# Kernel optimization log

Measured on AMD Instinct MI355X. Metric: run time of the kernel, lower is better.

Reference implementation:

```python
import jax, jax.numpy as jnp
import numpy as np


def _conv1d(x, w, b, stride=1, pad=0):
    # x: [B, Cin, L], w: [Cout, Cin, K] (torch OIH layout)
    y = jax.lax.conv_general_dilated(
        x, w, window_strides=(stride,), padding=[(pad, pad)],
        dimension_numbers=('NCH', 'OIH', 'NCH'))
    return y + b[None, :, None]


def setup_inputs() -> dict:
    key = jax.random.key(0)
    ks = jax.random.split(key, 8)
    B, M, C, Hf, Wf, Ho, Wo = 4, 112, 512, 13, 13, 16, 16
    return {
        'features_f': jax.random.normal(ks[0], (B, C, Hf, Wf), jnp.float32),   # cfp last feature map
        'oct_feats':  jax.random.normal(ks[1], (B, M, C, Ho, Wo), jnp.float32),  # per-slice last feature maps
        'conv1d_w':   jax.random.normal(ks[2], (64, 1024, 64), jnp.float32) * 0.02,
        'conv1d_b':   jnp.zeros((64,), jnp.float32),
        'convf_w':    jax.random.normal(ks[3], (13, 64, 5), jnp.float32) * 0.05,
        'convf_b':    jnp.zeros((13,), jnp.float32),
        'head_w':     jax.random.normal(ks[4], (3, 1536), jnp.float32) * 0.02,
        'head_b':     jnp.zeros((3,), jnp.float32),
    }


def reference(features_f, oct_feats, conv1d_w, conv1d_b, convf_w, convf_b, head_w, head_b):
    B, M, C, Ho, Wo = oct_feats.shape
    # per-slice global avg / max pools of encoder_o feature maps -> [B, M, C]
    fv = oct_feats.mean(axis=(3, 4))
    fv_max = oct_feats.max(axis=(3, 4))
    # slice attention: conv1d over slice axis on concatenated [B, 2C, M]
    x = jnp.concatenate([fv, fv_max], axis=2).transpose(0, 2, 1)
    slice_weights = jax.nn.sigmoid(_conv1d(x, conv1d_w, conv1d_b))  # [B, 64, M-63]
    # argmax-indexed per-channel gather: for each (b, c) pick the slice whose
    # pooled activation is largest, then copy that slice's [Ho, Wo] map.
    idx = jnp.argmax(fv, axis=1)          # [B, C]
    idx_max = jnp.argmax(fv_max, axis=1)  # [B, C]
    sel = jnp.take_along_axis(oct_feats, idx[:, None, :, None, None], axis=1)[:, 0]        # [B, C, Ho, Wo]
    sel_max = jnp.take_along_axis(oct_feats, idx_max[:, None, :, None, None], axis=1)[:, 0]
    feat_o_avg = sel.mean(axis=(2, 3))      # original applies avgpool to both selections
    feat_o_max = sel_max.mean(axis=(2, 3))
    feat_o = jnp.concatenate([feat_o_avg, feat_o_max], axis=1)  # [B, 1024]
    # fundus attention map r: [B, 13, 13], broadcast over C channels
    r = jax.nn.sigmoid(_conv1d(slice_weights, convf_w, convf_b, stride=4, pad=2))
    attended = features_f + r[:, None, :, :] * features_f
    feat_f = attended.mean(axis=(2, 3))     # [B, 512]
    feat = jnp.concatenate([feat_f, feat_o], axis=1)  # [B, 1536]
    # classification head (dropout is identity at inference): Linear(1536 -> 3)
    return feat @ head_w.T + head_b
```

## Files before the change

kernel.cpp:

```cpp
#include <hip/hip_runtime.h>
#include <hip/hip_bf16.h>
#include <math.h>

#define XB_OFF 0
#define FO_OFF 917504
#define AM_OFF 933888
#define SW_OFF 933888
#define RF_OFF 0
#define FT_OFF 933888

__global__ __launch_bounds__(256) void k_init(unsigned long long* __restrict__ am) {
    am[blockIdx.x * 256 + threadIdx.x] = 0ULL;
}

__global__ __launch_bounds__(256) void k_pool(const float* __restrict__ oct,
                                              __hip_bfloat16* __restrict__ xb,
                                              unsigned long long* __restrict__ am) {
    int wg = (blockIdx.x * 256 + threadIdx.x) >> 6;
    int lane = threadIdx.x & 63;
    const float4* p = (const float4*)(oct + (size_t)wg * 256);
    float4 v = p[lane];
    float s  = v.x + v.y + v.z + v.w;
    float mx = fmaxf(fmaxf(v.x, v.y), fmaxf(v.z, v.w));
#pragma unroll
    for (int off = 32; off >= 1; off >>= 1) {
        s  += __shfl_xor(s, off);
        mx  = fmaxf(mx, __shfl_xor(mx, off));
    }
    if (lane == 0) {
        int c  = wg & 511;
        int bm = wg >> 9;
        int m  = bm % 112;
        int b  = bm / 112;
        xb[((size_t)b * 1024 + c) * 112 + m]       = __float2bfloat16(s * (1.0f / 256.0f));
        xb[((size_t)b * 1024 + 512 + c) * 112 + m] = __float2bfloat16(mx);
        unsigned int u = __float_as_uint(mx);
        unsigned int key = (u & 0x80000000u) ? ~u : (u | 0x80000000u);
        unsigned long long pk = ((unsigned long long)key << 32) | (unsigned int)(111 - m);
        atomicMax(&am[b * 512 + c], pk);
    }
}

__global__ __launch_bounds__(256) void k_feato(const __hip_bfloat16* __restrict__ xb,
                                               const unsigned long long* __restrict__ am,
                                               float* __restrict__ fo) {
    int wid  = blockIdx.x * 4 + (threadIdx.x >> 6);
    int lane = threadIdx.x & 63;
    int b = wid >> 9, c = wid & 511;
    const __hip_bfloat16* fvrow = xb + ((size_t)b * 1024 + c) * 112;
    float v0 = (lane < 112)      ? __bfloat162float(fvrow[lane])      : -INFINITY;
    float v1 = (lane + 64 < 112) ? __bfloat162float(fvrow[lane + 64]) : -INFINITY;
    float mxf = fmaxf(v0, v1);
#pragma unroll
    for (int off = 32; off >= 1; off >>= 1)
        mxf = fmaxf(mxf, __shfl_xor(mxf, off));
    if (lane == 0) {
        int mstar = 111 - (int)(unsigned int)(am[b * 512 + c] & 0xFFFFFFFFULL);
        fo[b * 1024 + c]       = mxf;
        fo[b * 1024 + 512 + c] = __bfloat162float(fvrow[mstar]);
    }
}

__global__ __launch_bounds__(256) void k_conv(const __hip_bfloat16* __restrict__ xb,
                                              const float* __restrict__ w1,
                                              const float* __restrict__ b1,
                                              float* __restrict__ sw) {
    __shared__ unsigned int xs[256 * 61];
    __shared__ float red[4][25];
    int bx = blockIdx.x;
    int lh = bx & 1, co = (bx >> 1) & 63, b = bx >> 7;
    int t = threadIdx.x, wv = t >> 6, lane = t & 63;
    int l0u = lh * 12;
    float acc[25];
#pragma unroll
    for (int i = 0; i < 25; i++) acc[i] = 0.f;
    const unsigned int* gxb = (const unsigned int*)xb;
    for (int chunk = 0; chunk < 4; chunk++) {
        __syncthreads();
        for (int r = wv; r < 256; r += 4)
            if (lane < 56)
                xs[r * 61 + lane] = gxb[((size_t)b * 1024 + chunk * 256 + r) * 56 + lane];
        __syncthreads();
        int cil = wv * 64 + lane;
        int ci  = chunk * 256 + cil;
        const unsigned int* xu = xs + cil * 61 + l0u;
        float xf[88];
#pragma unroll
        for (int i = 0; i < 44; i++) {
            unsigned int u = xu[i];
            xf[2 * i]     = __uint_as_float(u << 16);
            xf[2 * i + 1] = __uint_as_float(u & 0xffff0000u);
        }
        const float* wrow = w1 + ((size_t)co * 1024 + ci) * 64;
#pragma unroll
        for (int kc = 0; kc < 4; kc++) {
            float ww[16];
#pragma unroll
            for (int j = 0; j < 16; j++) ww[j] = wrow[kc * 16 + j];
#pragma unroll
            for (int k = 0; k < 16; k++)
#pragma unroll
                for (int i = 0; i < 25; i++)
                    acc[i] += ww[k] * xf[kc * 16 + k + i];
        }
    }
#pragma unroll
    for (int i = 0; i < 25; i++) {
#pragma unroll
        for (int off = 32; off >= 1; off >>= 1)
            acc[i] += __shfl_xor(acc[i], off);
    }
    if (lane < 25) red[wv][lane] = acc[lane];
    __syncthreads();
    if (t < 25) {
        float s = red[0][t] + red[1][t] + red[2][t] + red[3][t] + b1[co];
        float sg = 1.f / (1.f + expf(-s));
        int l = lh * 24 + t;
        if (!(lh == 1 && t == 0))
            sw[(size_t)(b * 64 + co) * 49 + l] = sg;
    }
}

__global__ __launch_bounds__(256) void k_r(const float* __restrict__ sw,
                                           const float* __restrict__ cw,
                                           const float* __restrict__ cb,
                                           float* __restrict__ rf) {
    __shared__ float swl[3136];
    __shared__ float cwl[4160];
    int b = blockIdx.x, t = threadIdx.x;
    for (int i = t; i < 3136; i += 256) swl[i] = sw[b * 3136 + i];
    for (int i = t; i < 4160; i += 256) cwl[i] = cw[i];
    __syncthreads();
    if (t < 169) {
        int o = t / 13, l = t % 13;
        float s = cb[o];
        for (int i = 0; i < 64; i++) {
#pragma unroll
            for (int k = 0; k < 5; k++) {
                int pos = 4 * l + k - 2;
                if (pos >= 0 && pos < 49)
                    s += swl[i * 49 + pos] * cwl[(o * 64 + i) * 5 + k];
            }
        }
        rf[b * 169 + t] = 1.f + 1.f / (1.f + expf(-s));
    }
}

__global__ __launch_bounds__(256) void k_ff(const float* __restrict__ ff,
                                            const float* __restrict__ rf,
                                            float* __restrict__ feat) {
    __shared__ float r1[169];
    int b = blockIdx.x >> 3, cg = blockIdx.x & 7;
    int t = threadIdx.x, wv = t >> 6, lane = t & 63;
    if (t < 169) r1[t] = rf[b * 169 + t];
    __syncthreads();
#pragma unroll
    for (int j = 0; j < 16; j++) {
        int c = cg * 64 + wv * 16 + j;
        const float* row = ff + ((size_t)b * 512 + c) * 169;
        float s = row[lane] * r1[lane];
        if (lane + 64 < 169)  s += row[lane + 64]  * r1[lane + 64];
        if (lane + 128 < 169) s += row[lane + 128] * r1[lane + 128];
#pragma unroll
        for (int off = 32; off >= 1; off >>= 1) s += __shfl_xor(s, off);
        if (lane == 0) feat[b * 512 + c] = s * (1.0f / 169.0f);
    }
}

__global__ __launch_bounds__(256) void k_head(const float* __restrict__ feat,
                                              const float* __restrict__ fo,
                                              const float* __restrict__ hw,
                                              const float* __restrict__ hb,
                                              float* __restrict__ out) {
    __shared__ float red[4];
    int bj = blockIdx.x;
    int b = bj / 3, j = bj % 3;
    int t = threadIdx.x, wv = t >> 6, lane = t & 63;
    float s = 0.f;
#pragma unroll
    for (int rep = 0; rep < 6; rep++) {
        int i = rep * 256 + t;
        float fv = (i < 512) ? feat[b * 512 + i] : fo[b * 1024 + (i - 512)];
        s += fv * hw[j * 1536 + i];
    }
#pragma unroll
    for (int off = 32; off >= 1; off >>= 1) s += __shfl_xor(s, off);
    if (lane == 0) red[wv] = s;
    __syncthreads();
    if (t == 0)
        out[b * 3 + j] = red[0] + red[1] + red[2] + red[3] + hb[j];
}

extern "C" void kernel_launch(void* const* d_in, const int* in_sizes, int n_in,
                              void* d_out, int out_size, void* d_ws, size_t ws_size,
                              hipStream_t stream) {
    const float* ff  = (const float*)d_in[0];
    const float* oct = (const float*)d_in[1];
    const float* w1  = (const float*)d_in[2];
    const float* b1  = (const float*)d_in[3];
    const float* cw  = (const float*)d_in[4];
    const float* cb  = (const float*)d_in[5];
    const float* hw  = (const float*)d_in[6];
    const float* hb  = (const float*)d_in[7];
    float* out = (float*)d_out;
    char* ws = (char*)d_ws;
    __hip_bfloat16*     xb = (__hip_bfloat16*)(ws + XB_OFF);
    float*              fo = (float*)(ws + FO_OFF);
    unsigned long long* am = (unsigned long long*)(ws + AM_OFF);
    float*              sw = (float*)(ws + SW_OFF);
    float*              rf = (float*)(ws + RF_OFF);
    float*            feat = (float*)(ws + FT_OFF);

    hipLaunchKernelGGL(k_init,  dim3(8),     dim3(256), 0, stream, am);
    hipLaunchKernelGGL(k_pool,  dim3(57344), dim3(256), 0, stream, oct, xb, am);
    hipLaunchKernelGGL(k_feato, dim3(512),   dim3(256), 0, stream, xb, am, fo);
    hipLaunchKernelGGL(k_conv,  dim3(512),   dim3(256), 0, stream, xb, w1, b1, sw);
    hipLaunchKernelGGL(k_r,     dim3(4),     dim3(256), 0, stream, sw, cw, cb, rf);
    hipLaunchKernelGGL(k_ff,    dim3(32),    dim3(256), 0, stream, ff, rf, feat);
    hipLaunchKernelGGL(k_head,  dim3(12),    dim3(256), 0, stream, feat, fo, hw, hb, out);
}
```

Measured before the change: 466.4 us.

## Fuse pooling with argmax selection and merge tail kernels into one

Pooling now runs one block per (batch, channel) that loops over all slices, computing mean/max pools and the argmax-selected features in-block. This removes the atomic packed argmax, the init kernel and the separate selection kernel. The fundus attention, weighted feature pooling and linear head are fused into a single per-batch kernel. The aim is fewer launches and less atomic and intermediate traffic. The cost is a tail kernel running on only 4 blocks with strided per-thread loops.

```diff
diff --git a/kernel.cpp b/kernel.cpp
--- a/kernel.cpp
+++ b/kernel.cpp
@@ -4,61 +4,76 @@
 
 #define XB_OFF 0
 #define FO_OFF 917504
-#define AM_OFF 933888
 #define SW_OFF 933888
-#define RF_OFF 0
-#define FT_OFF 933888
-
-__global__ __launch_bounds__(256) void k_init(unsigned long long* __restrict__ am) {
-    am[blockIdx.x * 256 + threadIdx.x] = 0ULL;
-}
 
 __global__ __launch_bounds__(256) void k_pool(const float* __restrict__ oct,
                                               __hip_bfloat16* __restrict__ xb,
-                                              unsigned long long* __restrict__ am) {
-    int wg = (blockIdx.x * 256 + threadIdx.x) >> 6;
-    int lane = threadIdx.x & 63;
-    const float4* p = (const float4*)(oct + (size_t)wg * 256);
-    float4 v = p[lane];
-    float s  = v.x + v.y + v.z + v.w;
-    float mx = fmaxf(fmaxf(v.x, v.y), fmaxf(v.z, v.w));
-#pragma unroll
-    for (int off = 32; off >= 1; off >>= 1) {
-        s  += __shfl_xor(s, off);
-        mx  = fmaxf(mx, __shfl_xor(mx, off));
-    }
-    if (lane == 0) {
-        int c  = wg & 511;
-        int bm = wg >> 9;
-        int m  = bm % 112;
-        int b  = bm / 112;
-        xb[((size_t)b * 1024 + c) * 112 + m]       = __float2bfloat16(s * (1.0f / 256.0f));
-        xb[((size_t)b * 1024 + 512 + c) * 112 + m] = __float2bfloat16(mx);
-        unsigned int u = __float_as_uint(mx);
-        unsigned int key = (u & 0x80000000u) ? ~u : (u | 0x80000000u);
-        unsigned long long pk = ((unsigned long long)key << 32) | (unsigned int)(111 - m);
-        atomicMax(&am[b * 512 + c], pk);
-    }
-}
-
-__global__ __launch_bounds__(256) void k_feato(const __hip_bfloat16* __restrict__ xb,
-                                               const unsigned long long* __restrict__ am,
-                                               float* __restrict__ fo) {
-    int wid  = blockIdx.x * 4 + (threadIdx.x >> 6);
-    int lane = threadIdx.x & 63;
-    int b = wid >> 9, c = wid & 511;
-    const __hip_bfloat16* fvrow = xb + ((size_t)b * 1024 + c) * 112;
-    float v0 = (lane < 112)      ? __bfloat162float(fvrow[lane])      : -INFINITY;
-    float v1 = (lane + 64 < 112) ? __bfloat162float(fvrow[lane + 64]) : -INFINITY;
-    float mxf = fmaxf(v0, v1);
-#pragma unroll
-    for (int off = 32; off >= 1; off >>= 1)
-        mxf = fmaxf(mxf, __shfl_xor(mxf, off));
-    if (lane == 0) {
-        int mstar = 111 - (int)(unsigned int)(am[b * 512 + c] & 0xFFFFFFFFULL);
-        fo[b * 1024 + c]       = mxf;
-        fo[b * 1024 + 512 + c] = __bfloat162float(fvrow[mstar]);
-    }
+                                              float* __restrict__ fo) {
+    __shared__ unsigned int fvu[56];
+    __shared__ unsigned int fvmu[56];
+    __shared__ float s_bmx[4], s_bat[4], s_bfv[4];
+    __shared__ int   s_bm[4];
+    __hip_bfloat16* fvl  = (__hip_bfloat16*)fvu;
+    __hip_bfloat16* fvml = (__hip_bfloat16*)fvmu;
+    int b = blockIdx.x >> 9, c = blockIdx.x & 511;
+    int t = threadIdx.x, w = t >> 6, lane = t & 63;
+    int g = lane >> 4, p = lane & 15;
+    const float* base = oct + ((size_t)b * 112 * 512 + c) * 256;
+    float bmx = -INFINITY, bat = 0.f, bfv = -INFINITY;
+    int bm = 0;
+    for (int it = 0; it < 7; ++it) {
+        int m = w * 28 + it * 4 + g;
+        const float4* mp = (const float4*)(base + (size_t)m * (512 * 256));
+        float4 a0 = mp[p];
+        float4 a1 = mp[p + 16];
+        float4 a2 = mp[p + 32];
+        float4 a3 = mp[p + 48];
+        float s = (a0.x + a0.y + a0.z + a0.w) + (a1.x + a1.y + a1.z + a1.w)
+                + (a2.x + a2.y + a2.z + a2.w) + (a3.x + a3.y + a3.z + a3.w);
+        float mx = fmaxf(fmaxf(fmaxf(a0.x, a0.y), fmaxf(a0.z, a0.w)),
+                         fmaxf(fmaxf(a1.x, a1.y), fmaxf(a1.z, a1.w)));
+        mx = fmaxf(mx, fmaxf(fmaxf(fmaxf(a2.x, a2.y), fmaxf(a2.z, a2.w)),
+                             fmaxf(fmaxf(a3.x, a3.y), fmaxf(a3.z, a3.w))));
+#pragma unroll
+        for (int off = 1; off <= 8; off <<= 1) {
+            s  += __shfl_xor(s, off);
+            mx  = fmaxf(mx, __shfl_xor(mx, off));
+        }
+        float fv = s * (1.0f / 256.0f);
+        if (mx > bmx) { bmx = mx; bm = m; bat = fv; }
+        bfv = fmaxf(bfv, fv);
+        if (p == 0) {
+            fvl[m]  = __float2bfloat16(fv);
+            fvml[m] = __float2bfloat16(mx);
+        }
+    }
+#pragma unroll
+    for (int off = 16; off <= 32; off <<= 1) {
+        float omx = __shfl_xor(bmx, off);
+        int   om  = __shfl_xor(bm, off);
+        float oat = __shfl_xor(bat, off);
+        float obf = __shfl_xor(bfv, off);
+        if (omx > bmx || (omx == bmx && om < bm)) { bmx = omx; bm = om; bat = oat; }
+        bfv = fmaxf(bfv, obf);
+    }
+    if (lane == 0) { s_bmx[w] = bmx; s_bm[w] = bm; s_bat[w] = bat; s_bfv[w] = bfv; }
+    __syncthreads();
+    if (t == 0) {
+        float M = s_bmx[0], A = s_bat[0], F = s_bfv[0];
+        int   I = s_bm[0];
+        for (int w2 = 1; w2 < 4; ++w2) {
+            if (s_bmx[w2] > M || (s_bmx[w2] == M && s_bm[w2] < I)) {
+                M = s_bmx[w2]; I = s_bm[w2]; A = s_bat[w2];
+            }
+            F = fmaxf(F, s_bfv[w2]);
+        }
+        fo[b * 1024 + c]       = F;
+        fo[b * 1024 + 512 + c] = A;
+    }
+    unsigned int* xo  = (unsigned int*)(xb + (size_t)(b * 1024 + c) * 112);
+    unsigned int* xo2 = (unsigned int*)(xb + (size_t)(b * 1024 + 512 + c) * 112);
+    if (t < 56)                    xo[t]       = fvu[t];
+    else if (t >= 64 && t < 120)   xo2[t - 64] = fvmu[t - 64];
 }
 
 __global__ __launch_bounds__(256) void k_conv(const __hip_bfloat16* __restrict__ xb,
@@ -121,13 +136,20 @@
     }
 }
 
-__global__ __launch_bounds__(256) void k_r(const float* __restrict__ sw,
-                                           const float* __restrict__ cw,
-                                           const float* __restrict__ cb,
-                                           float* __restrict__ rf) {
+__global__ __launch_bounds__(256) void k_tail(const float* __restrict__ sw,
+                                              const float* __restrict__ cw,
+                                              const float* __restrict__ cb,
+                                              const float* __restrict__ ff,
+                                              const float* __restrict__ fo,
+                                              const float* __restrict__ hw,
+                                              const float* __restrict__ hb,
+                                              float* __restrict__ out) {
     __shared__ float swl[3136];
     __shared__ float cwl[4160];
-    int b = blockIdx.x, t = threadIdx.x;
+    __shared__ float rfl[169];
+    __shared__ float ffl[512];
+    __shared__ float hred[3][4];
+    int b = blockIdx.x, t = threadIdx.x, w = t >> 6, lane = t & 63;
     for (int i = t; i < 3136; i += 256) swl[i] = sw[b * 3136 + i];
     for (int i = t; i < 4160; i += 256) cwl[i] = cw[i];
     __syncthreads();
@@ -142,53 +164,43 @@
                     s += swl[i * 49 + pos] * cwl[(o * 64 + i) * 5 + k];
             }
         }
-        rf[b * 169 + t] = 1.f + 1.f / (1.f + expf(-s));
-    }
-}
-
-__global__ __launch_bounds__(256) void k_ff(const float* __restrict__ ff,
-                                            const float* __restrict__ rf,
-                                            float* __restrict__ feat) {
-    __shared__ float r1[169];
-    int b = blockIdx.x >> 3, cg = blockIdx.x & 7;
-    int t = threadIdx.x, wv = t >> 6, lane = t & 63;
-    if (t < 169) r1[t] = rf[b * 169 + t];
-    __syncthreads();
-#pragma unroll
-    for (int j = 0; j < 16; j++) {
-        int c = cg * 64 + wv * 16 + j;
-        const float* row = ff + ((size_t)b * 512 + c) * 169;
-        float s = row[lane] * r1[lane];
-        if (lane + 64 < 169)  s += row[lane + 64]  * r1[lane + 64];
-        if (lane + 128 < 169) s += row[lane + 128] * r1[lane + 128];
-#pragma unroll
-        for (int off = 32; off >= 1; off >>= 1) s += __shfl_xor(s, off);
-        if (lane == 0) feat[b * 512 + c] = s * (1.0f / 169.0f);
-    }
-}
-
-__global__ __launch_bounds__(256) void k_head(const float* __restrict__ feat,
-                                              const float* __restrict__ fo,
-                                              const float* __restrict__ hw,
-                                              const float* __restrict__ hb,
-                                              float* __restrict__ out) {
-    __shared__ float red[4];
-    int bj = blockIdx.x;
-    int b = bj / 3, j = bj % 3;
-    int t = threadIdx.x, wv = t >> 6, lane = t & 63;
-    float s = 0.f;
-#pragma unroll
-    for (int rep = 0; rep < 6; rep++) {
-        int i = rep * 256 + t;
-        float fv = (i < 512) ? feat[b * 512 + i] : fo[b * 1024 + (i - 512)];
-        s += fv * hw[j * 1536 + i];
-    }
-#pragma unroll
-    for (int off = 32; off >= 1; off >>= 1) s += __shfl_xor(s, off);
-    if (lane == 0) red[wv] = s;
-    __syncthreads();
-    if (t == 0)
-        out[b * 3 + j] = red[0] + red[1] + red[2] + red[3] + hb[j];
+        rfl[t] = 1.f + 1.f / (1.f + expf(-s));
+    }
+    __syncthreads();
+    {
+        float acc1 = 0.f, acc2 = 0.f;
+        const float* r1 = ff + ((size_t)b * 512 + t) * 169;
+        const float* r2 = r1 + 256 * 169;
+        for (int pidx = 0; pidx < 169; ++pidx) {
+            float rv = rfl[pidx];
+            acc1 += r1[pidx] * rv;
+            acc2 += r2[pidx] * rv;
+        }
+        ffl[t]       = acc1 * (1.0f / 169.0f);
+        ffl[t + 256] = acc2 * (1.0f / 169.0f);
+    }
+    __syncthreads();
+    {
+        float s0 = 0.f, s1 = 0.f, s2 = 0.f;
+#pragma unroll
+        for (int rep = 0; rep < 6; ++rep) {
+            int i = rep * 256 + t;
+            float fv = (i < 512) ? ffl[i] : fo[b * 1024 + (i - 512)];
+            s0 += fv * hw[i];
+            s1 += fv * hw[1536 + i];
+            s2 += fv * hw[3072 + i];
+        }
+#pragma unroll
+        for (int off = 32; off >= 1; off >>= 1) {
+            s0 += __shfl_xor(s0, off);
+            s1 += __shfl_xor(s1, off);
+            s2 += __shfl_xor(s2, off);
+        }
+        if (lane == 0) { hred[0][w] = s0; hred[1][w] = s1; hred[2][w] = s2; }
+    }
+    __syncthreads();
+    if (t < 3)
+        out[b * 3 + t] = hred[t][0] + hred[t][1] + hred[t][2] + hred[t][3] + hb[t];
 }
 
 extern "C" void kernel_launch(void* const* d_in, const int* in_sizes, int n_in,
@@ -204,18 +216,11 @@
     const float* hb  = (const float*)d_in[7];
     float* out = (float*)d_out;
     char* ws = (char*)d_ws;
-    __hip_bfloat16*     xb = (__hip_bfloat16*)(ws + XB_OFF);
-    float*              fo = (float*)(ws + FO_OFF);
-    unsigned long long* am = (unsigned long long*)(ws + AM_OFF);
-    float*              sw = (float*)(ws + SW_OFF);
-    float*              rf = (float*)(ws + RF_OFF);
-    float*            feat = (float*)(ws + FT_OFF);
-
-    hipLaunchKernelGGL(k_init,  dim3(8),     dim3(256), 0, stream, am);
-    hipLaunchKernelGGL(k_pool,  dim3(57344), dim3(256), 0, stream, oct, xb, am);
-    hipLaunchKernelGGL(k_feato, dim3(512),   dim3(256), 0, stream, xb, am, fo);
-    hipLaunchKernelGGL(k_conv,  dim3(512),   dim3(256), 0, stream, xb, w1, b1, sw);
-    hipLaunchKernelGGL(k_r,     dim3(4),     dim3(256), 0, stream, sw, cw, cb, rf);
-    hipLaunchKernelGGL(k_ff,    dim3(32),    dim3(256), 0, stream, ff, rf, feat);
-    hipLaunchKernelGGL(k_head,  dim3(12),    dim3(256), 0, stream, feat, fo, hw, hb, out);
-}
+    __hip_bfloat16* xb = (__hip_bfloat16*)(ws + XB_OFF);
+    float*          fo = (float*)(ws + FO_OFF);
+    float*          sw = (float*)(ws + SW_OFF);
+
+    hipLaunchKernelGGL(k_pool, dim3(2048), dim3(256), 0, stream, oct, xb, fo);
+    hipLaunchKernelGGL(k_conv, dim3(512),  dim3(256), 0, stream, xb, w1, b1, sw);
+    hipLaunchKernelGGL(k_tail, dim3(4),    dim3(256), 0, stream, sw, cw, cb, ff, fo, hw, hb, out);
+}
```

Result: slower. 476.1 us (+2.1%).

## Replace atomic argmax pooling with spilled pooled values and fuse tail kernels

Applied to the files above, without the earlier changes.

The pooling pass now writes both per-slice pooled values to workspace in fp32. A second kernel does a per-(b,c) wavefront argmax over the 112 slices, which replaces the atomic-based argmax and its init kernel. The r-map, fundus feature reduction and linear head are merged into one 4-block tail kernel, cutting two launches and the global round-trips between them. The cost is extra workspace traffic and a tail whose per-thread strided reads of the fundus features are uncoalesced and spread over only 4 blocks.

```diff
diff --git a/kernel.cpp b/kernel.cpp
--- a/kernel.cpp
+++ b/kernel.cpp
@@ -2,12 +2,70 @@
 #include <hip/hip_bf16.h>
 #include <math.h>
 
-#define XB_OFF 0
-#define FO_OFF 917504
-#define AM_OFF 933888
-#define SW_OFF 933888
-#define RF_OFF 0
-#define FT_OFF 933888
+#define XB_OFF  0
+#define FO_OFF  917504
+#define AM_OFF  933888
+#define SW_OFF  933888
+#define FVX_OFF 984064
+#define FVA_OFF 1901568
+#define SPILL_NEED (FVA_OFF + 917504)
+
+__global__ __launch_bounds__(256) void k_pool1(const float* __restrict__ oct,
+                                               __hip_bfloat16* __restrict__ xb,
+                                               float* __restrict__ fvx,
+                                               float* __restrict__ fva) {
+    int wg = (blockIdx.x * 256 + threadIdx.x) >> 6;
+    int lane = threadIdx.x & 63;
+    const float4* p = (const float4*)(oct + (size_t)wg * 256);
+    float4 v = p[lane];
+    float s  = v.x + v.y + v.z + v.w;
+    float mx = fmaxf(fmaxf(v.x, v.y), fmaxf(v.z, v.w));
+#pragma unroll
+    for (int off = 32; off >= 1; off >>= 1) {
+        s  += __shfl_xor(s, off);
+        mx  = fmaxf(mx, __shfl_xor(mx, off));
+    }
+    if (lane == 0) {
+        int c  = wg & 511;
+        int bm = wg >> 9;
+        int m  = bm % 112;
+        int b  = bm / 112;
+        float fv = s * (1.0f / 256.0f);
+        xb[((size_t)b * 1024 + c) * 112 + m]       = __float2bfloat16(fv);
+        xb[((size_t)b * 1024 + 512 + c) * 112 + m] = __float2bfloat16(mx);
+        fvx[((size_t)b * 512 + c) * 112 + m] = mx;
+        fva[((size_t)b * 512 + c) * 112 + m] = fv;
+    }
+}
+
+__global__ __launch_bounds__(256) void k_pool2(const float* __restrict__ fvx,
+                                               const float* __restrict__ fva,
+                                               float* __restrict__ fo) {
+    int wid  = blockIdx.x * 4 + (threadIdx.x >> 6);
+    int lane = threadIdx.x & 63;
+    int b = wid >> 9, c = wid & 511;
+    const float* kx = fvx + (size_t)wid * 112;
+    const float* va = fva + (size_t)wid * 112;
+    int m0 = lane, m1 = lane + 64;
+    float k0 = (m0 < 112) ? kx[m0] : -INFINITY;
+    float k1 = (m1 < 112) ? kx[m1] : -INFINITY;
+    float f0 = (m0 < 112) ? va[m0] : -INFINITY;
+    float f1 = (m1 < 112) ? va[m1] : -INFINITY;
+    float bk; int bm;
+    if (k1 > k0) { bk = k1; bm = m1; } else { bk = k0; bm = m0; }
+    float bf = fmaxf(f0, f1);
+#pragma unroll
+    for (int off = 32; off >= 1; off >>= 1) {
+        float ok = __shfl_xor(bk, off);
+        int   om = __shfl_xor(bm, off);
+        if (ok > bk || (ok == bk && om < bm)) { bk = ok; bm = om; }
+        bf = fmaxf(bf, __shfl_xor(bf, off));
+    }
+    if (lane == 0) {
+        fo[b * 1024 + c]       = bf;
+        fo[b * 1024 + 512 + c] = va[bm];
+    }
+}
 
 __global__ __launch_bounds__(256) void k_init(unsigned long long* __restrict__ am) {
     am[blockIdx.x * 256 + threadIdx.x] = 0ULL;
@@ -121,13 +179,20 @@
     }
 }
 
-__global__ __launch_bounds__(256) void k_r(const float* __restrict__ sw,
-                                           const float* __restrict__ cw,
-                                           const float* __restrict__ cb,
-                                           float* __restrict__ rf) {
+__global__ __launch_bounds__(256) void k_tail(const float* __restrict__ sw,
+                                              const float* __restrict__ cw,
+                                              const float* __restrict__ cb,
+                                              const float* __restrict__ ff,
+                                              const float* __restrict__ fo,
+                                              const float* __restrict__ hw,
+                                              const float* __restrict__ hb,
+                                              float* __restrict__ out) {
     __shared__ float swl[3136];
     __shared__ float cwl[4160];
-    int b = blockIdx.x, t = threadIdx.x;
+    __shared__ float rfl[169];
+    __shared__ float ffl[512];
+    __shared__ float hred[3][4];
+    int b = blockIdx.x, t = threadIdx.x, w = t >> 6, lane = t & 63;
     for (int i = t; i < 3136; i += 256) swl[i] = sw[b * 3136 + i];
     for (int i = t; i < 4160; i += 256) cwl[i] = cw[i];
     __syncthreads();
@@ -142,53 +207,43 @@
                     s += swl[i * 49 + pos] * cwl[(o * 64 + i) * 5 + k];
             }
         }
-        rf[b * 169 + t] = 1.f + 1.f / (1.f + expf(-s));
-    }
-}
-
-__global__ __launch_bounds__(256) void k_ff(const float* __restrict__ ff,
-                                            const float* __restrict__ rf,
-                                            float* __restrict__ feat) {
-    __shared__ float r1[169];
-    int b = blockIdx.x >> 3, cg = blockIdx.x & 7;
-    int t = threadIdx.x, wv = t >> 6, lane = t & 63;
-    if (t < 169) r1[t] = rf[b * 169 + t];
-    __syncthreads();
-#pragma unroll
-    for (int j = 0; j < 16; j++) {
-        int c = cg * 64 + wv * 16 + j;
-        const float* row = ff + ((size_t)b * 512 + c) * 169;
-        float s = row[lane] * r1[lane];
-        if (lane + 64 < 169)  s += row[lane + 64]  * r1[lane + 64];
-        if (lane + 128 < 169) s += row[lane + 128] * r1[lane + 128];
-#pragma unroll
-        for (int off = 32; off >= 1; off >>= 1) s += __shfl_xor(s, off);
-        if (lane == 0) feat[b * 512 + c] = s * (1.0f / 169.0f);
-    }
-}
-
-__global__ __launch_bounds__(256) void k_head(const float* __restrict__ feat,
-                                              const float* __restrict__ fo,
-                                              const float* __restrict__ hw,
-                                              const float* __restrict__ hb,
-                                              float* __restrict__ out) {
-    __shared__ float red[4];
-    int bj = blockIdx.x;
-    int b = bj / 3, j = bj % 3;
-    int t = threadIdx.x, wv = t >> 6, lane = t & 63;
-    float s = 0.f;
-#pragma unroll
-    for (int rep = 0; rep < 6; rep++) {
-        int i = rep * 256 + t;
-        float fv = (i < 512) ? feat[b * 512 + i] : fo[b * 1024 + (i - 512)];
-        s += fv * hw[j * 1536 + i];
-    }
-#pragma unroll
-    for (int off = 32; off >= 1; off >>= 1) s += __shfl_xor(s, off);
-    if (lane == 0) red[wv] = s;
-    __syncthreads();
-    if (t == 0)
-        out[b * 3 + j] = red[0] + red[1] + red[2] + red[3] + hb[j];
+        rfl[t] = 1.f + 1.f / (1.f + expf(-s));
+    }
+    __syncthreads();
+    {
+        float acc1 = 0.f, acc2 = 0.f;
+        const float* r1 = ff + ((size_t)b * 512 + t) * 169;
+        const float* r2 = r1 + 256 * 169;
+        for (int pidx = 0; pidx < 169; ++pidx) {
+            float rv = rfl[pidx];
+            acc1 += r1[pidx] * rv;
+            acc2 += r2[pidx] * rv;
+        }
+        ffl[t]       = acc1 * (1.0f / 169.0f);
+        ffl[t + 256] = acc2 * (1.0f / 169.0f);
+    }
+    __syncthreads();
+    {
+        float s0 = 0.f, s1 = 0.f, s2 = 0.f;
+#pragma unroll
+        for (int rep = 0; rep < 6; ++rep) {
+            int i = rep * 256 + t;
+            float fv = (i < 512) ? ffl[i] : fo[b * 1024 + (i - 512)];
+            s0 += fv * hw[i];
+            s1 += fv * hw[1536 + i];
+            s2 += fv * hw[3072 + i];
+        }
+#pragma unroll
+        for (int off = 32; off >= 1; off >>= 1) {
+            s0 += __shfl_xor(s0, off);
+            s1 += __shfl_xor(s1, off);
+            s2 += __shfl_xor(s2, off);
+        }
+        if (lane == 0) { hred[0][w] = s0; hred[1][w] = s1; hred[2][w] = s2; }
+    }
+    __syncthreads();
+    if (t < 3)
+        out[b * 3 + t] = hred[t][0] + hred[t][1] + hred[t][2] + hred[t][3] + hb[t];
 }
 
 extern "C" void kernel_launch(void* const* d_in, const int* in_sizes, int n_in,
@@ -208,14 +263,17 @@
     float*              fo = (float*)(ws + FO_OFF);
     unsigned long long* am = (unsigned long long*)(ws + AM_OFF);
     float*              sw = (float*)(ws + SW_OFF);
-    float*              rf = (float*)(ws + RF_OFF);
-    float*            feat = (float*)(ws + FT_OFF);
-
-    hipLaunchKernelGGL(k_init,  dim3(8),     dim3(256), 0, stream, am);
-    hipLaunchKernelGGL(k_pool,  dim3(57344), dim3(256), 0, stream, oct, xb, am);
-    hipLaunchKernelGGL(k_feato, dim3(512),   dim3(256), 0, stream, xb, am, fo);
-    hipLaunchKernelGGL(k_conv,  dim3(512),   dim3(256), 0, stream, xb, w1, b1, sw);
-    hipLaunchKernelGGL(k_r,     dim3(4),     dim3(256), 0, stream, sw, cw, cb, rf);
-    hipLaunchKernelGGL(k_ff,    dim3(32),    dim3(256), 0, stream, ff, rf, feat);
-    hipLaunchKernelGGL(k_head,  dim3(12),    dim3(256), 0, stream, feat, fo, hw, hb, out);
-}
+
+    if (ws_size >= (size_t)SPILL_NEED) {
+        float* fvx = (float*)(ws + FVX_OFF);
+        float* fva = (float*)(ws + FVA_OFF);
+        hipLaunchKernelGGL(k_pool1, dim3(57344), dim3(256), 0, stream, oct, xb, fvx, fva);
+        hipLaunchKernelGGL(k_pool2, dim3(512),   dim3(256), 0, stream, fvx, fva, fo);
+    } else {
+        hipLaunchKernelGGL(k_init,  dim3(8),     dim3(256), 0, stream, am);
+        hipLaunchKernelGGL(k_pool,  dim3(57344), dim3(256), 0, stream, oct, xb, am);
+        hipLaunchKernelGGL(k_feato, dim3(512),   dim3(256), 0, stream, xb, am, fo);
+    }
+    hipLaunchKernelGGL(k_conv, dim3(512), dim3(256), 0, stream, xb, w1, b1, sw);
+    hipLaunchKernelGGL(k_tail, dim3(4),   dim3(256), 0, stream, sw, cw, cb, ff, fo, hw, hb, out);
+}
```

New measurement: 466.6 us. No clear change (+0.0%).
